# Kernel optimization log

Measured on AMD Instinct MI355X. Metric: run time of the kernel, lower is better.

Reference implementation:

```python
import jax, jax.numpy as jnp
import numpy as np

N = 50000
E = 800000
NODE_F = 128
HID = 96
TEMP_F = 10


def setup_inputs() -> dict:
    key = jax.random.key(0)
    ks = jax.random.split(key, 10)
    x = jax.random.normal(ks[0], (N, NODE_F), dtype=jnp.float32)
    edge_index = jax.random.randint(ks[1], (2, E), 0, N, dtype=jnp.int64)
    temporal = jax.random.normal(ks[2], (N, TEMP_F), dtype=jnp.float32)
    # GCNConv: lin weight [in, out] (no bias in lin), separate bias [out]
    W_gcn = jax.random.normal(ks[3], (NODE_F, HID), dtype=jnp.float32) / np.sqrt(NODE_F)
    b_gcn = jnp.zeros((HID,), dtype=jnp.float32)
    W1 = jax.random.normal(ks[4], (HID + TEMP_F, HID), dtype=jnp.float32) / np.sqrt(HID + TEMP_F)
    b1 = jax.random.normal(ks[5], (HID,), dtype=jnp.float32) * 0.01
    W2 = jax.random.normal(ks[6], (HID + NODE_F, 1), dtype=jnp.float32) / np.sqrt(HID + NODE_F)
    b2 = jax.random.normal(ks[7], (1,), dtype=jnp.float32) * 0.01
    return {"x": x, "edge_index": edge_index, "temporal": temporal,
            "W_gcn": W_gcn, "b_gcn": b_gcn, "W1": W1, "b1": b1, "W2": W2, "b2": b2}


def _gcn_conv(x, edge_index, W, b):
    n = x.shape[0]
    loop = jnp.arange(n, dtype=edge_index.dtype)
    src = jnp.concatenate([edge_index[0], loop])  # [E+N]
    dst = jnp.concatenate([edge_index[1], loop])
    # symmetric normalization with self-loops (PyG gcn_norm)
    ones = jnp.ones(src.shape[0], dtype=x.dtype)
    deg = jax.ops.segment_sum(ones, dst, num_segments=n)
    dinv = jnp.where(deg > 0, jax.lax.rsqrt(deg), 0.0)
    norm = dinv[src] * dinv[dst]  # [E+N]
    h = x @ W  # [N, HID]
    msg = h[src] * norm[:, None]  # [E+N, HID] gather + scale
    out = jax.ops.segment_sum(msg, dst, num_segments=n)  # scatter-add
    return out + b


def reference(x, edge_index, temporal, W_gcn, b_gcn, W1, b1, W2, b2):
    h = jax.nn.relu(_gcn_conv(x, edge_index, W_gcn, b_gcn))  # [N, HID]
    h = jnp.concatenate([h, temporal], axis=-1)              # [N, HID+TEMP_F]
    h = jax.nn.relu(h @ W1 + b1)                             # [N, HID]
    h = jnp.concatenate([h, x], axis=-1)                     # [N, HID+NODE_F]
    return jax.nn.relu(h @ W2 + b2)                          # [N, 1]
```

## Files before the change

kernel.cpp:

```cpp
#include <hip/hip_runtime.h>
#include <hip/hip_bf16.h>

#define NN 50000
#define NPAD 50048
#define NE 800000
#define NF 128
#define HH 96
#define TF 10
#define Z1DIM (HH + TF)
#define ZK 128
#define NCH 4
#define CW 24
#define NBK 196
#define CAP 5120
#define EPB 8192

typedef __attribute__((ext_vector_type(8))) short short8;
typedef __attribute__((ext_vector_type(8))) unsigned short ushort8;
typedef __attribute__((ext_vector_type(4))) float f32x4;

__device__ __forceinline__ float bu2f(unsigned short u) {
    union { unsigned int i; float f; } c;
    c.i = ((unsigned int)u) << 16;
    return c.f;
}
__device__ __forceinline__ unsigned short f2bu(float f) {
    union { __hip_bfloat16 h; unsigned short u; } c;
    c.h = __float2bfloat16(f);
    return c.u;
}

__global__ void k_init(int* __restrict__ bcur, int* __restrict__ off) {
    int t = threadIdx.x;
    if (t < NBK) bcur[t] = t * CAP;
    if (t == 255) off[NN] = NE;
}

__global__ __launch_bounds__(256) void k_fillA(const int* __restrict__ ei,
                                               int* __restrict__ bcur,
                                               int* __restrict__ temp) {
    __shared__ int hist[NBK], base[NBK];
    const int t = threadIdx.x;
    for (int m = t; m < NBK; m += 256) hist[m] = 0;
    __syncthreads();
    const int e0 = blockIdx.x * EPB;
    const int ecap = min(e0 + EPB, NE);
    for (int e = e0 + t; e < ecap; e += 256) {
        int d = ei[NE + e];
        atomicAdd(&hist[d >> 8], 1);
    }
    __syncthreads();
    for (int m = t; m < NBK; m += 256) {
        int c = hist[m];
        base[m] = c ? atomicAdd(&bcur[m], c) : 0;
        hist[m] = 0;
    }
    __syncthreads();
    for (int e = e0 + t; e < ecap; e += 256) {
        int d = ei[NE + e], s = ei[e];
        int b = d >> 8;
        int r = atomicAdd(&hist[b], 1);
        temp[base[b] + r] = ((d & 255) << 16) | s;
    }
}

__global__ __launch_bounds__(256) void k_gscan(const int* __restrict__ bcur,
                                               int* __restrict__ gbase) {
    __shared__ int p[256];
    const int t = threadIdx.x;
    int sz = (t < NBK) ? (bcur[t] - t * CAP) : 0;
    p[t] = sz;
    __syncthreads();
#pragma unroll
    for (int d = 1; d < 256; d <<= 1) {
        int u = (t >= d) ? p[t - d] : 0;
        __syncthreads();
        p[t] += u;
        __syncthreads();
    }
    if (t < NBK) gbase[t] = p[t] - sz;
}

__global__ __launch_bounds__(256) void k_fillB(const int* __restrict__ temp,
                                               const int* __restrict__ bcur,
                                               const int* __restrict__ gbase,
                                               int* __restrict__ csr,
                                               int* __restrict__ off) {
    __shared__ int ls[256], lc[256];
    const int b = blockIdx.x, t = threadIdx.x;
    const int seg0 = b * CAP;
    const int m = bcur[b] - seg0;
    const int g0 = gbase[b];
    ls[t] = 0;
    __syncthreads();
    for (int k = t; k < m; k += 256) atomicAdd(&ls[temp[seg0 + k] >> 16], 1);
    __syncthreads();
    const int myc = ls[t];
    lc[t] = myc;
    __syncthreads();
#pragma unroll
    for (int d = 1; d < 256; d <<= 1) {
        int u = (t >= d) ? lc[t - d] : 0;
        __syncthreads();
        lc[t] += u;
        __syncthreads();
    }
    const int myoff = lc[t] - myc;
    __syncthreads();
    lc[t] = myoff;
    const int i = b * 256 + t;
    if (i < NN) off[i] = g0 + myoff;
    __syncthreads();
    for (int k = t; k < m; k += 256) {
        int v = temp[seg0 + k];
        int r = atomicAdd(&lc[v >> 16], 1);
        csr[g0 + r] = v & 0xFFFF;
    }
}

#define XBLK (NPAD * NF / 4 / 256)
#define WBLK (NF * HH / 4 / 256)
#define W1BLK (HH * ZK / 4 / 256)
#define ZTBLK (NPAD / 32)
#define ZPBLK 5
__global__ void k_prep(const float* __restrict__ x, const float* __restrict__ W,
                       const float* __restrict__ W1, const float* __restrict__ tmp,
                       unsigned short* __restrict__ xb, unsigned short* __restrict__ Wt,
                       unsigned short* __restrict__ Wt1, unsigned short* __restrict__ zb) {
    int b = blockIdx.x;
    if (b < XBLK) {
        int idx4 = (b * 256 + threadIdx.x) * 4;
        int row = idx4 >> 7;
        ushort4 v;
        if (row < NN) {
            float4 f = *(const float4*)(x + idx4);
            v.x = f2bu(f.x); v.y = f2bu(f.y); v.z = f2bu(f.z); v.w = f2bu(f.w);
        } else {
            v.x = v.y = v.z = v.w = 0;
        }
        *(ushort4*)(xb + idx4) = v;
    } else if (b < XBLK + WBLK) {
        int e = ((b - XBLK) * 256 + threadIdx.x) * 4;
        int n = e >> 7, k = e & 127;
        ushort4 v;
        v.x = f2bu(W[(k + 0) * HH + n]);
        v.y = f2bu(W[(k + 1) * HH + n]);
        v.z = f2bu(W[(k + 2) * HH + n]);
        v.w = f2bu(W[(k + 3) * HH + n]);
        *(ushort4*)(Wt + e) = v;
    } else if (b < XBLK + WBLK + W1BLK) {
        int e = ((b - XBLK - WBLK) * 256 + threadIdx.x) * 4;
        int n = e >> 7, k = e & 127;
        ushort4 v;
        v.x = (k + 0 < Z1DIM) ? f2bu(W1[(k + 0) * HH + n]) : (unsigned short)0;
        v.y = (k + 1 < Z1DIM) ? f2bu(W1[(k + 1) * HH + n]) : (unsigned short)0;
        v.z = (k + 2 < Z1DIM) ? f2bu(W1[(k + 2) * HH + n]) : (unsigned short)0;
        v.w = (k + 3 < Z1DIM) ? f2bu(W1[(k + 3) * HH + n]) : (unsigned short)0;
        *(ushort4*)(Wt1 + e) = v;
    } else if (b < XBLK + WBLK + W1BLK + ZTBLK) {
        int t4 = ((b - XBLK - WBLK - W1BLK) * 256 + threadIdx.x) * 4;
        int i = t4 >> 5, cc = t4 & 31;
        ushort4 v; v.x = v.y = v.z = v.w = 0;
        if (i < NN) {
            if (cc + 0 < TF) v.x = f2bu(tmp[(size_t)i * TF + cc + 0]);
            if (cc + 1 < TF) v.y = f2bu(tmp[(size_t)i * TF + cc + 1]);
            if (cc + 2 < TF) v.z = f2bu(tmp[(size_t)i * TF + cc + 2]);
            if (cc + 3 < TF) v.w = f2bu(tmp[(size_t)i * TF + cc + 3]);
        }
        *(ushort4*)(zb + (size_t)i * ZK + HH + cc) = v;
    } else {
        int t4 = ((b - XBLK - WBLK - W1BLK - ZTBLK) * 256 + threadIdx.x) * 4;
        if (t4 < (NPAD - NN) * HH) {
            int i = NN + t4 / HH, j = t4 % HH;
            ushort4 z; z.x = z.y = z.z = z.w = 0;
            *(ushort4*)(zb + (size_t)i * ZK + j) = z;
        }
    }
}

__global__ __launch_bounds__(256) void k_gemm(const unsigned short* __restrict__ xb,
                                              const unsigned short* __restrict__ Wt,
                                              const int* __restrict__ off,
                                              unsigned short* __restrict__ hp_c) {
    const int wave = threadIdx.x >> 6;
    const int lane = threadIdx.x & 63;
    const int quad = lane >> 4;
    const int l16 = lane & 15;
    const int Mbase = blockIdx.x * 64 + wave * 16;

    const unsigned short* arow = xb + (size_t)(Mbase + l16) * NF + quad * 8;
    const unsigned short* brow = Wt + (size_t)l16 * NF + quad * 8;

    f32x4 acc[6] = {};
#pragma unroll
    for (int ks = 0; ks < 4; ++ks) {
        short8 a = *(const short8*)(arow + ks * 32);
#pragma unroll
        for (int nt = 0; nt < 6; ++nt) {
            short8 bfrag = *(const short8*)(brow + (size_t)nt * 16 * NF + ks * 32);
            acc[nt] = __builtin_amdgcn_mfma_f32_16x16x32_bf16(a, bfrag, acc[nt], 0, 0, 0);
        }
    }
    const int r0 = Mbase + quad * 4;
    float dv[4];
#pragma unroll
    for (int k = 0; k < 4; ++k) {
        int r = r0 + k;
        dv[k] = (r < NN) ? rsqrtf((float)(off[r + 1] - off[r]) + 1.f) : 0.f;
    }
#pragma unroll
    for (int nt = 0; nt < 6; ++nt) {
        int n = nt * 16 + l16;
        int c = n / CW, jj = n - c * CW;
        unsigned short* dst = hp_c + (size_t)c * NN * CW + jj;
#pragma unroll
        for (int k = 0; k < 4; ++k)
            if (r0 + k < NN) dst[(size_t)(r0 + k) * CW] = f2bu(acc[nt][k] * dv[k]);
    }
}

#define RPC 586
#define AGGB (4 * RPC)
__global__ __launch_bounds__(256) void k_agg(const unsigned short* __restrict__ hp_c,
                                             const int* __restrict__ off,
                                             const int* __restrict__ csr,
                                             const float* __restrict__ bg,
                                             unsigned short* __restrict__ zb) {
    const int b = blockIdx.x;
    const int slot = b & 7;
    const int c = slot >> 1;
    const int r = (b >> 3) * 2 + (slot & 1);
    const int item = r * 256 + threadIdx.x;
    if (item >= NN * 3) return;
    const int i = item / 3;
    const int q = item - i * 3;
    const unsigned short* base = hp_c + (size_t)c * NN * CW + q * 8;

    ushort8 sv = *(const ushort8*)(base + (size_t)i * CW);
    float a0 = bu2f(sv[0]), a1 = bu2f(sv[1]), a2 = bu2f(sv[2]), a3 = bu2f(sv[3]);
    float a4 = bu2f(sv[4]), a5 = bu2f(sv[5]), a6 = bu2f(sv[6]), a7 = bu2f(sv[7]);

    int idx = off[i];
    const int end = off[i + 1];
    const float dv = rsqrtf((float)(end - idx) + 1.f);
    for (; idx + 1 < end; idx += 2) {
        int s0 = csr[idx], s1 = csr[idx + 1];
        ushort8 v0 = *(const ushort8*)(base + (size_t)s0 * CW);
        ushort8 v1 = *(const ushort8*)(base + (size_t)s1 * CW);
        a0 += bu2f(v0[0]) + bu2f(v1[0]);
        a1 += bu2f(v0[1]) + bu2f(v1[1]);
        a2 += bu2f(v0[2]) + bu2f(v1[2]);
        a3 += bu2f(v0[3]) + bu2f(v1[3]);
        a4 += bu2f(v0[4]) + bu2f(v1[4]);
        a5 += bu2f(v0[5]) + bu2f(v1[5]);
        a6 += bu2f(v0[6]) + bu2f(v1[6]);
        a7 += bu2f(v0[7]) + bu2f(v1[7]);
    }
    if (idx < end) {
        ushort8 v0 = *(const ushort8*)(base + (size_t)csr[idx] * CW);
        a0 += bu2f(v0[0]); a1 += bu2f(v0[1]); a2 += bu2f(v0[2]); a3 += bu2f(v0[3]);
        a4 += bu2f(v0[4]); a5 += bu2f(v0[5]); a6 += bu2f(v0[6]); a7 += bu2f(v0[7]);
    }
    const int j = c * CW + q * 8;
    ushort8 o;
    o[0] = f2bu(fmaxf(fmaf(dv, a0, bg[j + 0]), 0.f));
    o[1] = f2bu(fmaxf(fmaf(dv, a1, bg[j + 1]), 0.f));
    o[2] = f2bu(fmaxf(fmaf(dv, a2, bg[j + 2]), 0.f));
    o[3] = f2bu(fmaxf(fmaf(dv, a3, bg[j + 3]), 0.f));
    o[4] = f2bu(fmaxf(fmaf(dv, a4, bg[j + 4]), 0.f));
    o[5] = f2bu(fmaxf(fmaf(dv, a5, bg[j + 5]), 0.f));
    o[6] = f2bu(fmaxf(fmaf(dv, a6, bg[j + 6]), 0.f));
    o[7] = f2bu(fmaxf(fmaf(dv, a7, bg[j + 7]), 0.f));
    *(ushort8*)(zb + (size_t)i * ZK + j) = o;
}

__global__ __launch_bounds__(256) void k_mlp2(const unsigned short* __restrict__ zb,
                                              const unsigned short* __restrict__ Wt1,
                                              const float* __restrict__ b1,
                                              const float* __restrict__ W2,
                                              const float* __restrict__ b2,
                                              const float* __restrict__ x,
                                              float* __restrict__ out) {
    const int wave = threadIdx.x >> 6;
    const int lane = threadIdx.x & 63;
    const int quad = lane >> 4;
    const int l16 = lane & 15;
    const int Mbase = blockIdx.x * 64 + wave * 16;

    const unsigned short* arow = zb + (size_t)(Mbase + l16) * ZK + quad * 8;
    const unsigned short* brow = Wt1 + (size_t)l16 * ZK + quad * 8;

    f32x4 acc[6] = {};
#pragma unroll
    for (int ks = 0; ks < 4; ++ks) {
        short8 a = *(const short8*)(arow + ks * 32);
#pragma unroll
        for (int nt = 0; nt < 6; ++nt) {
            short8 bfrag = *(const short8*)(brow + (size_t)nt * 16 * ZK + ks * 32);
            acc[nt] = __builtin_amdgcn_mfma_f32_16x16x32_bf16(a, bfrag, acc[nt], 0, 0, 0);
        }
    }
    float bb[6], wa[6];
#pragma unroll
    for (int nt = 0; nt < 6; ++nt) {
        int c = nt * 16 + l16;
        bb[nt] = b1[c];
        wa[nt] = W2[c];
    }
    float wx[8];
#pragma unroll
    for (int m = 0; m < 8; ++m) wx[m] = W2[HH + l16 * 8 + m];
    const float bias2 = b2[0];

#pragma unroll
    for (int reg = 0; reg < 4; ++reg) {
        const int r = Mbase + quad * 4 + reg;
        float p = 0.f;
#pragma unroll
        for (int nt = 0; nt < 6; ++nt)
            p = fmaf(fmaxf(acc[nt][reg] + bb[nt], 0.f), wa[nt], p);
        if (r < NN) {
            const float4 xa = *(const float4*)(x + (size_t)r * NF + l16 * 8);
            const float4 xc = *(const float4*)(x + (size_t)r * NF + l16 * 8 + 4);
            p = fmaf(xa.x, wx[0], p); p = fmaf(xa.y, wx[1], p);
            p = fmaf(xa.z, wx[2], p); p = fmaf(xa.w, wx[3], p);
            p = fmaf(xc.x, wx[4], p); p = fmaf(xc.y, wx[5], p);
            p = fmaf(xc.z, wx[6], p); p = fmaf(xc.w, wx[7], p);
        }
#pragma unroll
        for (int m = 1; m < 16; m <<= 1) p += __shfl_xor(p, m, 64);
        if (l16 == 0 && r < NN) out[r] = fmaxf(p + bias2, 0.f);
    }
}

extern "C" void kernel_launch(void* const* d_in, const int* in_sizes, int n_in,
                              void* d_out, int out_size, void* d_ws, size_t ws_size,
                              hipStream_t stream) {
    const float* x   = (const float*)d_in[0];
    const int*   ei  = (const int*)d_in[1];
    const float* tmp = (const float*)d_in[2];
    const float* Wg  = (const float*)d_in[3];
    const float* bg  = (const float*)d_in[4];
    const float* W1  = (const float*)d_in[5];
    const float* b1  = (const float*)d_in[6];
    const float* W2  = (const float*)d_in[7];
    const float* b2  = (const float*)d_in[8];
    float* out = (float*)d_out;

    char* base = (char*)d_ws;
    int* off  = (int*)base;
    int* bcur = off + 65536;
    int* gbase = bcur + 256;
    int* csr  = gbase + 256;
    unsigned short* xb = (unsigned short*)(base + ((size_t)4 << 20) + 262144);
    unsigned short* Wt = xb + (size_t)NPAD * NF;
    unsigned short* hp_c = Wt + NF * HH;
    unsigned short* Wt1 = hp_c + (size_t)NN * HH;
    unsigned short* zb = Wt1 + HH * ZK;
    int* temp = (int*)zb;

    k_init <<<1, 256, 0, stream>>>(bcur, off);
    k_fillA<<<(NE + EPB - 1) / EPB, 256, 0, stream>>>(ei, bcur, temp);
    k_gscan<<<1, 256, 0, stream>>>(bcur, gbase);
    k_fillB<<<NBK, 256, 0, stream>>>(temp, bcur, gbase, csr, off);
    k_prep <<<XBLK + WBLK + W1BLK + ZTBLK + ZPBLK, 256, 0, stream>>>(x, Wg, W1, tmp, xb, Wt, Wt1, zb);
    k_gemm <<<NPAD / 64, 256, 0, stream>>>(xb, Wt, off, hp_c);
    k_agg  <<<AGGB, 256, 0, stream>>>(hp_c, off, csr, bg, zb);
    k_mlp2 <<<NPAD / 64, 256, 0, stream>>>(zb, Wt1, b1, W2, b2, x, out);
}
```

Before: 195.3 us.

## Fuse x bf16 conversion into GEMM and shrink CSR indices to 16-bit

Drops the separate pass converting x to bf16 and instead converts fp32 x rows on the fly inside the GEMM A-fragment load. CSR neighbour indices are stored as 16-bit values instead of 32-bit, halving index traffic in the aggregation. This removes a full read/write of the node feature matrix and reduces gather bandwidth, at the cost of wider fp32 loads in the GEMM and reliance on node ids fitting in 16 bits.

```diff
diff --git a/kernel.cpp b/kernel.cpp
--- a/kernel.cpp
+++ b/kernel.cpp
@@ -84,7 +84,7 @@
 __global__ __launch_bounds__(256) void k_fillB(const int* __restrict__ temp,
                                                const int* __restrict__ bcur,
                                                const int* __restrict__ gbase,
-                                               int* __restrict__ csr,
+                                               unsigned short* __restrict__ csr,
                                                int* __restrict__ off) {
     __shared__ int ls[256], lc[256];
     const int b = blockIdx.x, t = threadIdx.x;
@@ -114,33 +114,21 @@
     for (int k = t; k < m; k += 256) {
         int v = temp[seg0 + k];
         int r = atomicAdd(&lc[v >> 16], 1);
-        csr[g0 + r] = v & 0xFFFF;
-    }
-}
-
-#define XBLK (NPAD * NF / 4 / 256)
+        csr[g0 + r] = (unsigned short)(v & 0xFFFF);
+    }
+}
+
 #define WBLK (NF * HH / 4 / 256)
 #define W1BLK (HH * ZK / 4 / 256)
 #define ZTBLK (NPAD / 32)
 #define ZPBLK 5
-__global__ void k_prep(const float* __restrict__ x, const float* __restrict__ W,
+__global__ void k_prep(const float* __restrict__ W,
                        const float* __restrict__ W1, const float* __restrict__ tmp,
-                       unsigned short* __restrict__ xb, unsigned short* __restrict__ Wt,
+                       unsigned short* __restrict__ Wt,
                        unsigned short* __restrict__ Wt1, unsigned short* __restrict__ zb) {
     int b = blockIdx.x;
-    if (b < XBLK) {
-        int idx4 = (b * 256 + threadIdx.x) * 4;
-        int row = idx4 >> 7;
-        ushort4 v;
-        if (row < NN) {
-            float4 f = *(const float4*)(x + idx4);
-            v.x = f2bu(f.x); v.y = f2bu(f.y); v.z = f2bu(f.z); v.w = f2bu(f.w);
-        } else {
-            v.x = v.y = v.z = v.w = 0;
-        }
-        *(ushort4*)(xb + idx4) = v;
-    } else if (b < XBLK + WBLK) {
-        int e = ((b - XBLK) * 256 + threadIdx.x) * 4;
+    if (b < WBLK) {
+        int e = (b * 256 + threadIdx.x) * 4;
         int n = e >> 7, k = e & 127;
         ushort4 v;
         v.x = f2bu(W[(k + 0) * HH + n]);
@@ -148,8 +136,8 @@
         v.z = f2bu(W[(k + 2) * HH + n]);
         v.w = f2bu(W[(k + 3) * HH + n]);
         *(ushort4*)(Wt + e) = v;
-    } else if (b < XBLK + WBLK + W1BLK) {
-        int e = ((b - XBLK - WBLK) * 256 + threadIdx.x) * 4;
+    } else if (b < WBLK + W1BLK) {
+        int e = ((b - WBLK) * 256 + threadIdx.x) * 4;
         int n = e >> 7, k = e & 127;
         ushort4 v;
         v.x = (k + 0 < Z1DIM) ? f2bu(W1[(k + 0) * HH + n]) : (unsigned short)0;
@@ -157,8 +145,8 @@
         v.z = (k + 2 < Z1DIM) ? f2bu(W1[(k + 2) * HH + n]) : (unsigned short)0;
         v.w = (k + 3 < Z1DIM) ? f2bu(W1[(k + 3) * HH + n]) : (unsigned short)0;
         *(ushort4*)(Wt1 + e) = v;
-    } else if (b < XBLK + WBLK + W1BLK + ZTBLK) {
-        int t4 = ((b - XBLK - WBLK - W1BLK) * 256 + threadIdx.x) * 4;
+    } else if (b < WBLK + W1BLK + ZTBLK) {
+        int t4 = ((b - WBLK - W1BLK) * 256 + threadIdx.x) * 4;
         int i = t4 >> 5, cc = t4 & 31;
         ushort4 v; v.x = v.y = v.z = v.w = 0;
         if (i < NN) {
@@ -169,7 +157,7 @@
         }
         *(ushort4*)(zb + (size_t)i * ZK + HH + cc) = v;
     } else {
-        int t4 = ((b - XBLK - WBLK - W1BLK - ZTBLK) * 256 + threadIdx.x) * 4;
+        int t4 = ((b - WBLK - W1BLK - ZTBLK) * 256 + threadIdx.x) * 4;
         if (t4 < (NPAD - NN) * HH) {
             int i = NN + t4 / HH, j = t4 % HH;
             ushort4 z; z.x = z.y = z.z = z.w = 0;
@@ -178,7 +166,7 @@
     }
 }
 
-__global__ __launch_bounds__(256) void k_gemm(const unsigned short* __restrict__ xb,
+__global__ __launch_bounds__(256) void k_gemm(const float* __restrict__ x,
                                               const unsigned short* __restrict__ Wt,
                                               const int* __restrict__ off,
                                               unsigned short* __restrict__ hp_c) {
@@ -187,14 +175,24 @@
     const int quad = lane >> 4;
     const int l16 = lane & 15;
     const int Mbase = blockIdx.x * 64 + wave * 16;
-
-    const unsigned short* arow = xb + (size_t)(Mbase + l16) * NF + quad * 8;
+    const int row = Mbase + l16;
+    const bool valid = row < NN;
+
+    const float* xr = x + (size_t)row * NF + quad * 8;
     const unsigned short* brow = Wt + (size_t)l16 * NF + quad * 8;
 
     f32x4 acc[6] = {};
 #pragma unroll
     for (int ks = 0; ks < 4; ++ks) {
-        short8 a = *(const short8*)(arow + ks * 32);
+        short8 a = {};
+        if (valid) {
+            float4 f0 = *(const float4*)(xr + ks * 32);
+            float4 f1 = *(const float4*)(xr + ks * 32 + 4);
+            a[0] = (short)f2bu(f0.x); a[1] = (short)f2bu(f0.y);
+            a[2] = (short)f2bu(f0.z); a[3] = (short)f2bu(f0.w);
+            a[4] = (short)f2bu(f1.x); a[5] = (short)f2bu(f1.y);
+            a[6] = (short)f2bu(f1.z); a[7] = (short)f2bu(f1.w);
+        }
 #pragma unroll
         for (int nt = 0; nt < 6; ++nt) {
             short8 bfrag = *(const short8*)(brow + (size_t)nt * 16 * NF + ks * 32);
@@ -223,7 +221,7 @@
 #define AGGB (4 * RPC)
 __global__ __launch_bounds__(256) void k_agg(const unsigned short* __restrict__ hp_c,
                                              const int* __restrict__ off,
-                                             const int* __restrict__ csr,
+                                             const unsigned short* __restrict__ csr,
                                              const float* __restrict__ bg,
                                              unsigned short* __restrict__ zb) {
     const int b = blockIdx.x;
@@ -351,20 +349,19 @@
     int* off  = (int*)base;
     int* bcur = off + 65536;
     int* gbase = bcur + 256;
-    int* csr  = gbase + 256;
-    unsigned short* xb = (unsigned short*)(base + ((size_t)4 << 20) + 262144);
-    unsigned short* Wt = xb + (size_t)NPAD * NF;
-    unsigned short* hp_c = Wt + NF * HH;
-    unsigned short* Wt1 = hp_c + (size_t)NN * HH;
-    unsigned short* zb = Wt1 + HH * ZK;
+    unsigned short* csr = (unsigned short*)(gbase + 256);
+    unsigned short* Wt  = (unsigned short*)(base + ((size_t)4 << 20));
+    unsigned short* Wt1 = Wt + NF * HH;
+    unsigned short* hp_c = Wt1 + HH * ZK;
+    unsigned short* zb = hp_c + (size_t)NN * HH;
     int* temp = (int*)zb;
 
     k_init <<<1, 256, 0, stream>>>(bcur, off);
     k_fillA<<<(NE + EPB - 1) / EPB, 256, 0, stream>>>(ei, bcur, temp);
     k_gscan<<<1, 256, 0, stream>>>(bcur, gbase);
     k_fillB<<<NBK, 256, 0, stream>>>(temp, bcur, gbase, csr, off);
-    k_prep <<<XBLK + WBLK + W1BLK + ZTBLK + ZPBLK, 256, 0, stream>>>(x, Wg, W1, tmp, xb, Wt, Wt1, zb);
-    k_gemm <<<NPAD / 64, 256, 0, stream>>>(xb, Wt, off, hp_c);
+    k_prep <<<WBLK + W1BLK + ZTBLK + ZPBLK, 256, 0, stream>>>(Wg, W1, tmp, Wt, Wt1, zb);
+    k_gemm <<<NPAD / 64, 256, 0, stream>>>(x, Wt, off, hp_c);
     k_agg  <<<AGGB, 256, 0, stream>>>(hp_c, off, csr, bg, zb);
     k_mlp2 <<<NPAD / 64, 256, 0, stream>>>(zb, Wt1, b1, W2, b2, x, out);
 }
```

Measured after the change: 189.2 us. 1.03x faster.
